# Optimization experiments

Hardware: AMD Instinct MI355X
Metric: run time of the kernel (lower is better)

Reference implementation:

```python
import jax, jax.numpy as jnp
import numpy as np

E, S, G, H, O = 50000, 16, 64, 256, 16


def _mlp(x, W0, b0, W1, b1, W2, b2):
    # x: [..., 2] -> [..., out]
    x = jax.nn.relu(x @ W0 + b0)
    x = jax.nn.relu(x @ W1 + b1)
    return x @ W2 + b2


def setup_inputs() -> dict:
    key = jax.random.key(0)
    ks = jax.random.split(key, 9)
    ob = jax.random.normal(ks[0], (E, S, 3), dtype=jnp.float32)
    action = jax.random.randint(ks[1], (E, S), 0, O).astype(jnp.int64)
    graph_ids = jnp.sort(jax.random.randint(ks[2], (E,), 0, G)).astype(jnp.int32)
    def lin(k, fin, fout):
        return jax.random.normal(k, (fin, fout), dtype=jnp.float32) / jnp.sqrt(jnp.float32(fin))
    return {
        "ob": ob, "action": action, "graph_ids": graph_ids,
        "aW0": lin(ks[3], 2, H), "ab0": jnp.zeros((H,), jnp.float32),
        "aW1": lin(ks[4], H, H), "ab1": jnp.zeros((H,), jnp.float32),
        "aW2": lin(ks[5], H, O), "ab2": jnp.zeros((O,), jnp.float32),
        "cW0": lin(ks[6], 2, H), "cb0": jnp.zeros((H,), jnp.float32),
        "cW1": lin(ks[7], H, H), "cb1": jnp.zeros((H,), jnp.float32),
        "cW2": lin(ks[8], H, 1), "cb2": jnp.zeros((1,), jnp.float32),
    }


def reference(ob, action, graph_ids, aW0, ab0, aW1, ab1, aW2, ab2,
              cW0, cb0, cW1, cb1, cW2, cb2):
    num_edges = ob.shape[0]
    # edge_mask: torch `ob.select(2,0).long() == 0` (truncation toward zero)
    edge_mask = ob[..., 0].astype(jnp.int32) == 0            # [E,S] bool
    mf = edge_mask.astype(ob.dtype)                          # [E,S]
    h = ob[..., 1:3]                                         # [E,S,2]

    # Actor logits over all (edge,sample); mask replaces gather/scatter
    logits = _mlp(h, aW0, ab0, aW1, ab1, aW2, ab2)           # [E,S,O]
    logp = jax.nn.log_softmax(logits, axis=-1)               # [E,S,O]

    # log-prob of given actions, scattered to zeros outside the mask
    alp = jnp.take_along_axis(logp, action[..., None], axis=-1)[..., 0]
    action_log_probs = alp * mf                              # [E,S]

    # critic edge values, scattered to zeros outside the mask
    vals = _mlp(h, cW0, cb0, cW1, cb1, cW2, cb2)[..., 0] * mf  # [E,S]

    # entropy averaged over masked (subgraph) entries only
    ent = -jnp.sum(jnp.exp(logp) * logp, axis=-1)            # [E,S]
    avg_entropy = jnp.sum(ent * mf) / jnp.sum(mf)

    # sum_efeat: per-graph segment sum over edges, divided by num_edges
    value_preds = jax.ops.segment_sum(vals, graph_ids, num_segments=G) / num_edges  # [G,S]

    return action_log_probs, avg_entropy, value_preds, edge_mask
```

## Files before the change

kernel.cpp:

```cpp
#include <hip/hip_runtime.h>
#include <stdint.h>


typedef __attribute__((ext_vector_type(8))) short bf16x8;
typedef __attribute__((ext_vector_type(4))) float f32x4;
typedef __attribute__((ext_vector_type(4))) uint32_t u32x4;

#define NROWS    800000
#define NCHUNK   12500
#define OUT_ENT  800000
#define OUT_VP   800001
#define OUT_MASK 801025

#define SWZ(row) ((((row) & 7) << 4) ^ (((row) & 16) << 1))

__device__ __forceinline__ short f2bf(float x) {
  union { float f; uint32_t u; } v; v.f = x;
  return (short)(uint16_t)((v.u + 0x7FFFu + ((v.u >> 16) & 1u)) >> 16);
}
__device__ __forceinline__ float bf2f(short h) {
  union { uint32_t u; float f; } v; v.u = ((uint32_t)(uint16_t)h) << 16;
  return v.f;
}
template <int C>
__device__ __forceinline__ float dppf(float x) {
  int r = __builtin_amdgcn_update_dpp(0, __builtin_bit_cast(int, x), C, 0xF, 0xF, true);
  return __builtin_bit_cast(float, r);
}
__device__ __forceinline__ float red16_sum(float x) {
  x += dppf<0xB1>(x); x += dppf<0x4E>(x); x += dppf<0x124>(x); x += dppf<0x128>(x); return x;
}
__device__ __forceinline__ float red16_max(float x) {
  x = fmaxf(x, dppf<0xB1>(x)); x = fmaxf(x, dppf<0x4E>(x));
  x = fmaxf(x, dppf<0x124>(x)); x = fmaxf(x, dppf<0x128>(x)); return x;
}
__device__ __forceinline__ uint32_t cvt_pk_bf16(float a, float b) {
  uint32_t r; asm("v_cvt_pk_bf16_f32 %0, %1, %2" : "=v"(r) : "v"(a), "v"(b)); return r;
}

__global__ void zero_kernel(float* out, float* wsf) {
  int t = threadIdx.x + blockIdx.x * blockDim.x;
  for (int i = t; i < 1025; i += 1024) out[OUT_ENT + i] = 0.0f;
  if (t == 0) { wsf[0] = 0.0f; wsf[1] = 0.0f; }
}
__global__ void final_kernel(float* out, const float* wsf) {
  if (threadIdx.x == 0 && blockIdx.x == 0)
    out[OUT_ENT] = (wsf[1] > 0.0f) ? (wsf[0] / wsf[1]) : 0.0f;
}

#define A_ACT1 0
#define A_ACT2 32768
#define A_W2H  65536
#define A_W0   73728
#define A_B0   75776
#define A_OB   76800
#define A_SZ   78848

__global__ void __launch_bounds__(512, 2) ac_actor(
    const float* __restrict__ ob, const int* __restrict__ action,
    const float* __restrict__ aW0, const float* __restrict__ ab0,
    const float* __restrict__ aW1, const float* __restrict__ ab1,
    const float* __restrict__ aW2, const float* __restrict__ ab2,
    float* __restrict__ out, float* __restrict__ wsf)
{
  extern __shared__ char smem[];
  float* w0buf = (float*)(smem + A_W0);
  float* b0buf = (float*)(smem + A_B0);
  float* obufA = (float*)(smem + A_OB);
  const f32x4* w04 = (const f32x4*)(smem + A_W0);
  const f32x4* b04 = (const f32x4*)(smem + A_B0);
  __shared__ float went[8], wmf[8];

  const int tid = threadIdx.x, lane = tid & 63, wave = tid >> 6;
  const int l15 = lane & 15, l4 = lane >> 4;

  w0buf[tid] = aW0[tid];
  if (tid < 256) b0buf[tid] = ab0[tid];
  for (int id = tid; id < 4096; id += 512) {
    int n = id >> 8, k = id & 255;
    *(short*)(smem + A_W2H + n * 512 + ((k * 2) ^ SWZ(n))) = f2bf(aW2[k * 16 + n]);
  }
  const int colbase = wave * 32;
  float b1lane[2] = { ab1[colbase + l15], ab1[colbase + 16 + l15] };
  float b2lane = ab2[l15];
  bf16x8 bh[2][8];
  #pragma unroll
  for (int ct = 0; ct < 2; ++ct) {
    const int n = colbase + ct * 16 + l15;
    #pragma unroll
    for (int ks = 0; ks < 8; ++ks) {
      const int k0 = ks * 32 + 8 * l4;
      bf16x8 h8;
      #pragma unroll
      for (int j = 0; j < 8; ++j) h8[j] = f2bf(aW1[(k0 + j) * 256 + n]);
      bh[ct][ks] = h8;
    }
  }
  const int c0 = blockIdx.x, stride = gridDim.x;
  float sob = 0.0f;
  if (tid < 192) { obufA[tid] = ob[c0 * 192 + tid]; }
  { int cn = c0 + stride; if (cn < NCHUNK && tid < 192) sob = ob[cn * 192 + tid]; }
  __syncthreads();

  float entacc = 0.0f, mfacc = 0.0f;
  int buf = 0;
  for (int c = c0; c < NCHUNK; c += stride, buf ^= 1) {
    const int row0 = c * 64;
    const float* ocur = obufA + buf * 256;
    float* onxt = (float*)(obufA + (buf ^ 1) * 256);

    if (tid < 64) out[OUT_MASK + row0 + tid] = ((int)ocur[tid * 3] == 0) ? 1.0f : 0.0f;
    {
      const int kb = tid & 31;
      f32x4 wa0 = w04[kb * 2], wa1 = w04[kb * 2 + 1];
      f32x4 wb0 = w04[64 + kb * 2], wb1 = w04[64 + kb * 2 + 1];
      f32x4 ba0 = b04[kb * 2], ba1 = b04[kb * 2 + 1];
      #pragma unroll
      for (int i = 0; i < 4; ++i) {
        int row = wave * 2 + 16 * i + (lane >> 5);
        float h0 = ocur[row * 3 + 1], h1 = ocur[row * 3 + 2];
        f32x4 va, vb;
        #pragma unroll
        for (int j = 0; j < 4; ++j) {
          va[j] = fmaxf(fmaf(h0, wa0[j], fmaf(h1, wb0[j], ba0[j])), 0.0f);
          vb[j] = fmaxf(fmaf(h0, wa1[j], fmaf(h1, wb1[j], ba1[j])), 0.0f);
        }
        u32x4 v;
        v[0] = cvt_pk_bf16(va[0], va[1]);
        v[1] = cvt_pk_bf16(va[2], va[3]);
        v[2] = cvt_pk_bf16(vb[0], vb[1]);
        v[3] = cvt_pk_bf16(vb[2], vb[3]);
        *(u32x4*)(smem + A_ACT1 + row * 512 + ((kb * 16) ^ SWZ(row))) = v;
      }
    }
    if (tid < 192) onxt[tid] = sob;
    { int c2 = c + 2 * stride; if (c2 < NCHUNK && tid < 192) sob = ob[c2 * 192 + tid]; }
    __syncthreads();

    const bool evn = (l15 & 1) == 0;
    #pragma unroll 1
    for (int rtp = 0; rtp < 2; ++rtp) {
      f32x4 acc[2][2];
      #pragma unroll
      for (int h = 0; h < 2; ++h)
        #pragma unroll
        for (int ct = 0; ct < 2; ++ct) acc[h][ct] = (f32x4){0.f, 0.f, 0.f, 0.f};
      const int rA0 = rtp * 32 + l15, rA1 = rA0 + 16;
      #pragma unroll
      for (int ks = 0; ks < 8; ++ks) {
        const int cb = ks * 64 + 16 * l4;
        bf16x8 a0 = *(const bf16x8*)(smem + A_ACT1 + rA0 * 512 + (cb ^ SWZ(rA0)));
        bf16x8 a1 = *(const bf16x8*)(smem + A_ACT1 + rA1 * 512 + (cb ^ SWZ(rA1)));
        acc[0][0] = __builtin_amdgcn_mfma_f32_16x16x32_bf16(a0, bh[0][ks], acc[0][0], 0, 0, 0);
        acc[0][1] = __builtin_amdgcn_mfma_f32_16x16x32_bf16(a0, bh[1][ks], acc[0][1], 0, 0, 0);
        acc[1][0] = __builtin_amdgcn_mfma_f32_16x16x32_bf16(a1, bh[0][ks], acc[1][0], 0, 0, 0);
        acc[1][1] = __builtin_amdgcn_mfma_f32_16x16x32_bf16(a1, bh[1][ks], acc[1][1], 0, 0, 0);
      }
      #pragma unroll
      for (int ct = 0; ct < 2; ++ct) {
        const int colb = (colbase + ct * 16 + (l15 & ~1)) * 2;
        #pragma unroll
        for (int r = 0; r < 4; ++r) {
          float v0 = fmaxf(acc[0][ct][r] + b1lane[ct], 0.0f);
          float v1 = fmaxf(acc[1][ct][r] + b1lane[ct], 0.0f);
          float n0 = dppf<0xB1>(v0), n1 = dppf<0xB1>(v1);
          uint32_t w = cvt_pk_bf16(evn ? v0 : n1, evn ? n0 : v1);
          int rr = rtp * 32 + (evn ? 0 : 16) + 4 * l4 + r;
          *(uint32_t*)(smem + A_ACT2 + rr * 512 + (colb ^ SWZ(rr))) = w;
        }
      }
    }
    __syncthreads();

    if (wave < 4) {
      const int rowA = wave * 16 + l15;
      const int swA = SWZ(rowA), swW = SWZ(l15);
      f32x4 ae = {0.f,0.f,0.f,0.f}, ao = {0.f,0.f,0.f,0.f};
      #pragma unroll
      for (int ks = 0; ks < 8; ks += 2) {
        const int cb0 = ks * 64 + 16 * l4, cb1 = cb0 + 64;
        bf16x8 a0 = *(const bf16x8*)(smem + A_ACT2 + rowA * 512 + (cb0 ^ swA));
        bf16x8 a1 = *(const bf16x8*)(smem + A_ACT2 + rowA * 512 + (cb1 ^ swA));
        bf16x8 w0f = *(const bf16x8*)(smem + A_W2H + l15 * 512 + (cb0 ^ swW));
        bf16x8 w1f = *(const bf16x8*)(smem + A_W2H + l15 * 512 + (cb1 ^ swW));
        ae = __builtin_amdgcn_mfma_f32_16x16x32_bf16(a0, w0f, ae, 0, 0, 0);
        ao = __builtin_amdgcn_mfma_f32_16x16x32_bf16(a1, w1f, ao, 0, 0, 0);
      }
      #pragma unroll
      for (int r = 0; r < 4; ++r) {
        const int rl = wave * 16 + 4 * l4 + r;
        float x = ae[r] + ao[r] + b2lane;
        float m = red16_max(x);
        float e = __expf(x - m);
        float s = red16_sum(e);
        float t = red16_sum(e * (x - m));
        float ls = __logf(s);
        float mfr = ((int)ob[(row0 + rl) * 3] == 0) ? 1.0f : 0.0f;
        int av = action[row0 + rl];
        if (l15 == av) out[row0 + rl] = (x - m - ls) * mfr;
        if (l15 == 0) { entacc += (ls - t / s) * mfr; mfacc += mfr; }
      }
    }
  }
  #pragma unroll
  for (int d = 1; d < 64; d <<= 1) { entacc += __shfl_xor(entacc, d); mfacc += __shfl_xor(mfacc, d); }
  if (lane == 0) { went[wave] = entacc; wmf[wave] = mfacc; }
  __syncthreads();
  if (tid == 0) {
    float e = 0.f, m = 0.f;
    #pragma unroll
    for (int i = 0; i < 8; ++i) { e += went[i]; m += wmf[i]; }
    atomicAdd(&wsf[0], e); atomicAdd(&wsf[1], m);
  }
}

#define C_ACT1 0
#define C_W0   32768
#define C_B0   34816
#define C_OB   35840
#define C_VB   37888
#define C_SZ   39936

__global__ void __launch_bounds__(512, 2) ac_critic(
    const float* __restrict__ ob, const int* __restrict__ graph_ids,
    const float* __restrict__ cW0, const float* __restrict__ cb0,
    const float* __restrict__ cW1, const float* __restrict__ cb1,
    const float* __restrict__ cW2, const float* __restrict__ cb2,
    float* __restrict__ out)
{
  extern __shared__ char smem[];
  float* w0buf = (float*)(smem + C_W0);
  float* b0buf = (float*)(smem + C_B0);
  float* obufA = (float*)(smem + C_OB);
  float* vbuf  = (float*)(smem + C_VB);
  const f32x4* w04 = (const f32x4*)(smem + C_W0);
  const f32x4* b04 = (const f32x4*)(smem + C_B0);

  const int tid = threadIdx.x, lane = tid & 63, wave = tid >> 6;
  const int l15 = lane & 15, l4 = lane >> 4;

  w0buf[tid] = cW0[tid];
  if (tid < 256) b0buf[tid] = cb0[tid];
  const float cb2v = cb2[0];
  const int colbase = wave * 32;
  float b1lane[2] = { cb1[colbase + l15], cb1[colbase + 16 + l15] };
  const float w2c0 = cW2[colbase + l15];
  const float w2c1 = cW2[colbase + 16 + l15];

  bf16x8 bh[2][8];
  #pragma unroll
  for (int ct = 0; ct < 2; ++ct) {
    const int n = colbase + ct * 16 + l15;
    #pragma unroll
    for (int ks = 0; ks < 8; ++ks) {
      const int k0 = ks * 32 + 8 * l4;
      bf16x8 h8;
      #pragma unroll
      for (int j = 0; j < 8; ++j) h8[j] = f2bf(cW1[(k0 + j) * 256 + n]);
      bh[ct][ks] = h8;
    }
  }
  const int c0 = blockIdx.x, stride = gridDim.x;
  float sob = 0.0f;
  if (tid < 192) { obufA[tid] = ob[c0 * 192 + tid]; }
  { int cn = c0 + stride; if (cn < NCHUNK && tid < 192) sob = ob[cn * 192 + tid]; }
  __syncthreads();

  int buf = 0;
  for (int c = c0; c < NCHUNK; c += stride, buf ^= 1) {
    const float* ocur = obufA + buf * 256;
    float* onxt = (float*)(obufA + (buf ^ 1) * 256);

    {
      const int kb = tid & 31;
      f32x4 wa0 = w04[kb * 2], wa1 = w04[kb * 2 + 1];
      f32x4 wb0 = w04[64 + kb * 2], wb1 = w04[64 + kb * 2 + 1];
      f32x4 ba0 = b04[kb * 2], ba1 = b04[kb * 2 + 1];
      #pragma unroll
      for (int i = 0; i < 4; ++i) {
        int row = wave * 2 + 16 * i + (lane >> 5);
        float h0 = ocur[row * 3 + 1], h1 = ocur[row * 3 + 2];
        f32x4 va, vb;
        #pragma unroll
        for (int j = 0; j < 4; ++j) {
          va[j] = fmaxf(fmaf(h0, wa0[j], fmaf(h1, wb0[j], ba0[j])), 0.0f);
          vb[j] = fmaxf(fmaf(h0, wa1[j], fmaf(h1, wb1[j], ba1[j])), 0.0f);
        }
        u32x4 v;
        v[0] = cvt_pk_bf16(va[0], va[1]);
        v[1] = cvt_pk_bf16(va[2], va[3]);
        v[2] = cvt_pk_bf16(vb[0], vb[1]);
        v[3] = cvt_pk_bf16(vb[2], vb[3]);
        *(u32x4*)(smem + C_ACT1 + row * 512 + ((kb * 16) ^ SWZ(row))) = v;
      }
    }
    if (tid < 192) onxt[tid] = sob;
    { int c2 = c + 2 * stride; if (c2 < NCHUNK && tid < 192) sob = ob[c2 * 192 + tid]; }
    __syncthreads();

    float o0w0 = 0.0f;
    if (wave == 0) o0w0 = ocur[lane * 3];

    #pragma unroll 1
    for (int rtp = 0; rtp < 2; ++rtp) {
      f32x4 acc[2][2];
      #pragma unroll
      for (int h = 0; h < 2; ++h)
        #pragma unroll
        for (int ct = 0; ct < 2; ++ct) acc[h][ct] = (f32x4){0.f, 0.f, 0.f, 0.f};
      const int rA0 = rtp * 32 + l15, rA1 = rA0 + 16;
      #pragma unroll
      for (int ks = 0; ks < 8; ++ks) {
        const int cb = ks * 64 + 16 * l4;
        bf16x8 a0 = *(const bf16x8*)(smem + C_ACT1 + rA0 * 512 + (cb ^ SWZ(rA0)));
        bf16x8 a1 = *(const bf16x8*)(smem + C_ACT1 + rA1 * 512 + (cb ^ SWZ(rA1)));
        acc[0][0] = __builtin_amdgcn_mfma_f32_16x16x32_bf16(a0, bh[0][ks], acc[0][0], 0, 0, 0);
        acc[0][1] = __builtin_amdgcn_mfma_f32_16x16x32_bf16(a0, bh[1][ks], acc[0][1], 0, 0, 0);
        acc[1][0] = __builtin_amdgcn_mfma_f32_16x16x32_bf16(a1, bh[0][ks], acc[1][0], 0, 0, 0);
        acc[1][1] = __builtin_amdgcn_mfma_f32_16x16x32_bf16(a1, bh[1][ks], acc[1][1], 0, 0, 0);
      }
      #pragma unroll
      for (int h = 0; h < 2; ++h) {
        #pragma unroll
        for (int r = 0; r < 4; ++r) {
          float p = fmaxf(acc[h][0][r] + b1lane[0], 0.0f) * w2c0
                  + fmaxf(acc[h][1][r] + b1lane[1], 0.0f) * w2c1;
          p = red16_sum(p);
          if (l15 == 0) vbuf[wave * 64 + rtp * 32 + h * 16 + 4 * l4 + r] = p;
        }
      }
    }
    __syncthreads();

    if (wave == 0) {
      float v = 0.0f;
      #pragma unroll
      for (int w = 0; w < 8; ++w) v += vbuf[w * 64 + lane];
      if ((int)o0w0 == 0) {
        int g = graph_ids[c * 4 + (lane >> 4)];
        atomicAdd(&out[OUT_VP + g * 16 + (lane & 15)], (v + cb2v) * (1.0f / 50000.0f));
      }
    }
  }
}

extern "C" void kernel_launch(void* const* d_in, const int* in_sizes, int n_in,
                              void* d_out, int out_size, void* d_ws, size_t ws_size,
                              hipStream_t stream) {
  const float* ob     = (const float*)d_in[0];
  const int*   action = (const int*)d_in[1];
  const int*   gids   = (const int*)d_in[2];
  const float* aW0 = (const float*)d_in[3],  *ab0 = (const float*)d_in[4];
  const float* aW1 = (const float*)d_in[5],  *ab1 = (const float*)d_in[6];
  const float* aW2 = (const float*)d_in[7],  *ab2 = (const float*)d_in[8];
  const float* cW0 = (const float*)d_in[9],  *cb0 = (const float*)d_in[10];
  const float* cW1 = (const float*)d_in[11], *cb1 = (const float*)d_in[12];
  const float* cW2 = (const float*)d_in[13], *cb2 = (const float*)d_in[14];
  float* out = (float*)d_out;
  float* wsf = (float*)d_ws;

  zero_kernel<<<2, 512, 0, stream>>>(out, wsf);
  ac_actor<<<512, 512, A_SZ, stream>>>(ob, action, aW0, ab0, aW1, ab1, aW2, ab2, out, wsf);
  ac_critic<<<512, 512, C_SZ, stream>>>(ob, gids, cW0, cb0, cW1, cb1, cW2, cb2, out);
  final_kernel<<<1, 64, 0, stream>>>(out, wsf);
}
```

Before: 502.6 us.

## Merge actor and critic kernels into one launch with role-split blocks

```diff
diff --git a/kernel.cpp b/kernel.cpp
--- a/kernel.cpp
+++ b/kernel.cpp
@@ -48,41 +48,61 @@
     out[OUT_ENT] = (wsf[1] > 0.0f) ? (wsf[0] / wsf[1]) : 0.0f;
 }
 
-#define A_ACT1 0
-#define A_ACT2 32768
-#define A_W2H  65536
-#define A_W0   73728
-#define A_B0   75776
-#define A_OB   76800
-#define A_SZ   78848
-
-__global__ void __launch_bounds__(512, 2) ac_actor(
+#define L_ACT1 0
+#define L_ACT2 32768
+#define L_W2H  65536
+#define L_W0   73728
+#define L_B0   75776
+#define L_OB   76800
+#define L_SZ   78848
+
+__global__ void __launch_bounds__(512, 2) ac_main(
     const float* __restrict__ ob, const int* __restrict__ action,
+    const int* __restrict__ graph_ids,
     const float* __restrict__ aW0, const float* __restrict__ ab0,
     const float* __restrict__ aW1, const float* __restrict__ ab1,
     const float* __restrict__ aW2, const float* __restrict__ ab2,
+    const float* __restrict__ cW0, const float* __restrict__ cb0,
+    const float* __restrict__ cW1, const float* __restrict__ cb1,
+    const float* __restrict__ cW2, const float* __restrict__ cb2,
     float* __restrict__ out, float* __restrict__ wsf)
 {
   extern __shared__ char smem[];
-  float* w0buf = (float*)(smem + A_W0);
-  float* b0buf = (float*)(smem + A_B0);
-  float* obufA = (float*)(smem + A_OB);
-  const f32x4* w04 = (const f32x4*)(smem + A_W0);
-  const f32x4* b04 = (const f32x4*)(smem + A_B0);
+  float* w0buf = (float*)(smem + L_W0);
+  float* b0buf = (float*)(smem + L_B0);
+  float* obufA = (float*)(smem + L_OB);
+  float* vbuf  = (float*)(smem + L_ACT2);
+  const f32x4* w04 = (const f32x4*)(smem + L_W0);
+  const f32x4* b04 = (const f32x4*)(smem + L_B0);
   __shared__ float went[8], wmf[8];
+
+  const int b = blockIdx.x;
+  const int role = (b >> 8) & 1;
+  const int pid  = (b & 255) | ((b >> 9) << 8);
+  const int stride = 512;
 
   const int tid = threadIdx.x, lane = tid & 63, wave = tid >> 6;
   const int l15 = lane & 15, l4 = lane >> 4;
 
-  w0buf[tid] = aW0[tid];
-  if (tid < 256) b0buf[tid] = ab0[tid];
-  for (int id = tid; id < 4096; id += 512) {
-    int n = id >> 8, k = id & 255;
-    *(short*)(smem + A_W2H + n * 512 + ((k * 2) ^ SWZ(n))) = f2bf(aW2[k * 16 + n]);
+  const float* W0s = role ? cW0 : aW0;
+  const float* B0s = role ? cb0 : ab0;
+  const float* W1s = role ? cW1 : aW1;
+  const float* B1s = role ? cb1 : ab1;
+
+  w0buf[tid] = W0s[tid];
+  if (tid < 256) b0buf[tid] = B0s[tid];
+  if (!role) {
+    for (int id = tid; id < 4096; id += 512) {
+      int n = id >> 8, k = id & 255;
+      *(short*)(smem + L_W2H + n * 512 + ((k * 2) ^ SWZ(n))) = f2bf(aW2[k * 16 + n]);
+    }
   }
   const int colbase = wave * 32;
-  float b1lane[2] = { ab1[colbase + l15], ab1[colbase + 16 + l15] };
-  float b2lane = ab2[l15];
+  float b1lane[2] = { B1s[colbase + l15], B1s[colbase + 16 + l15] };
+  float b2lane = 0.0f, w2c0 = 0.0f, w2c1 = 0.0f, cb2v = 0.0f;
+  if (!role) b2lane = ab2[l15];
+  else { w2c0 = cW2[colbase + l15]; w2c1 = cW2[colbase + 16 + l15]; cb2v = cb2[0]; }
+
   bf16x8 bh[2][8];
   #pragma unroll
   for (int ct = 0; ct < 2; ++ct) {
@@ -92,24 +112,24 @@
       const int k0 = ks * 32 + 8 * l4;
       bf16x8 h8;
       #pragma unroll
-      for (int j = 0; j < 8; ++j) h8[j] = f2bf(aW1[(k0 + j) * 256 + n]);
+      for (int j = 0; j < 8; ++j) h8[j] = f2bf(W1s[(k0 + j) * 256 + n]);
       bh[ct][ks] = h8;
     }
   }
-  const int c0 = blockIdx.x, stride = gridDim.x;
   float sob = 0.0f;
-  if (tid < 192) { obufA[tid] = ob[c0 * 192 + tid]; }
-  { int cn = c0 + stride; if (cn < NCHUNK && tid < 192) sob = ob[cn * 192 + tid]; }
+  if (tid < 192) { obufA[tid] = ob[pid * 192 + tid]; }
+  { int cn = pid + stride; if (cn < NCHUNK && tid < 192) sob = ob[cn * 192 + tid]; }
   __syncthreads();
 
   float entacc = 0.0f, mfacc = 0.0f;
   int buf = 0;
-  for (int c = c0; c < NCHUNK; c += stride, buf ^= 1) {
+  for (int c = pid; c < NCHUNK; c += stride, buf ^= 1) {
     const int row0 = c * 64;
     const float* ocur = obufA + buf * 256;
     float* onxt = (float*)(obufA + (buf ^ 1) * 256);
 
-    if (tid < 64) out[OUT_MASK + row0 + tid] = ((int)ocur[tid * 3] == 0) ? 1.0f : 0.0f;
+    if (!role && tid < 64)
+      out[OUT_MASK + row0 + tid] = ((int)ocur[tid * 3] == 0) ? 1.0f : 0.0f;
     {
       const int kb = tid & 31;
       f32x4 wa0 = w04[kb * 2], wa1 = w04[kb * 2 + 1];
@@ -130,12 +150,15 @@
         v[1] = cvt_pk_bf16(va[2], va[3]);
         v[2] = cvt_pk_bf16(vb[0], vb[1]);
         v[3] = cvt_pk_bf16(vb[2], vb[3]);
-        *(u32x4*)(smem + A_ACT1 + row * 512 + ((kb * 16) ^ SWZ(row))) = v;
+        *(u32x4*)(smem + L_ACT1 + row * 512 + ((kb * 16) ^ SWZ(row))) = v;
       }
     }
     if (tid < 192) onxt[tid] = sob;
     { int c2 = c + 2 * stride; if (c2 < NCHUNK && tid < 192) sob = ob[c2 * 192 + tid]; }
     __syncthreads();
+
+    float o0w0 = 0.0f;
+    if (role && wave == 0) o0w0 = ocur[lane * 3];
 
     const bool evn = (l15 & 1) == 0;
     #pragma unroll 1
@@ -144,52 +167,68 @@
       #pragma unroll
       for (int h = 0; h < 2; ++h)
         #pragma unroll
-        for (int ct = 0; ct < 2; ++ct) acc[h][ct] = (f32x4){0.f, 0.f, 0.f, 0.f};
+        for (int ct = 0; ct < 2; ++ct)
+          acc[h][ct] = (f32x4){b1lane[ct], b1lane[ct], b1lane[ct], b1lane[ct]};
       const int rA0 = rtp * 32 + l15, rA1 = rA0 + 16;
       #pragma unroll
       for (int ks = 0; ks < 8; ++ks) {
         const int cb = ks * 64 + 16 * l4;
-        bf16x8 a0 = *(const bf16x8*)(smem + A_ACT1 + rA0 * 512 + (cb ^ SWZ(rA0)));
-        bf16x8 a1 = *(const bf16x8*)(smem + A_ACT1 + rA1 * 512 + (cb ^ SWZ(rA1)));
+        bf16x8 a0 = *(const bf16x8*)(smem + L_ACT1 + rA0 * 512 + (cb ^ SWZ(rA0)));
+        bf16x8 a1 = *(const bf16x8*)(smem + L_ACT1 + rA1 * 512 + (cb ^ SWZ(rA1)));
         acc[0][0] = __builtin_amdgcn_mfma_f32_16x16x32_bf16(a0, bh[0][ks], acc[0][0], 0, 0, 0);
         acc[0][1] = __builtin_amdgcn_mfma_f32_16x16x32_bf16(a0, bh[1][ks], acc[0][1], 0, 0, 0);
         acc[1][0] = __builtin_amdgcn_mfma_f32_16x16x32_bf16(a1, bh[0][ks], acc[1][0], 0, 0, 0);
         acc[1][1] = __builtin_amdgcn_mfma_f32_16x16x32_bf16(a1, bh[1][ks], acc[1][1], 0, 0, 0);
       }
-      #pragma unroll
-      for (int ct = 0; ct < 2; ++ct) {
-        const int colb = (colbase + ct * 16 + (l15 & ~1)) * 2;
-        #pragma unroll
-        for (int r = 0; r < 4; ++r) {
-          float v0 = fmaxf(acc[0][ct][r] + b1lane[ct], 0.0f);
-          float v1 = fmaxf(acc[1][ct][r] + b1lane[ct], 0.0f);
-          float n0 = dppf<0xB1>(v0), n1 = dppf<0xB1>(v1);
-          uint32_t w = cvt_pk_bf16(evn ? v0 : n1, evn ? n0 : v1);
-          int rr = rtp * 32 + (evn ? 0 : 16) + 4 * l4 + r;
-          *(uint32_t*)(smem + A_ACT2 + rr * 512 + (colb ^ SWZ(rr))) = w;
+      if (!role) {
+        #pragma unroll
+        for (int ct = 0; ct < 2; ++ct) {
+          const int colb = (colbase + ct * 16 + (l15 & ~1)) * 2;
+          #pragma unroll
+          for (int r = 0; r < 4; ++r) {
+            float v0 = fmaxf(acc[0][ct][r], 0.0f);
+            float v1 = fmaxf(acc[1][ct][r], 0.0f);
+            float n0 = dppf<0xB1>(v0), n1 = dppf<0xB1>(v1);
+            uint32_t w = cvt_pk_bf16(evn ? v0 : n1, evn ? n0 : v1);
+            int rr = rtp * 32 + (evn ? 0 : 16) + 4 * l4 + r;
+            *(uint32_t*)(smem + L_ACT2 + rr * 512 + (colb ^ SWZ(rr))) = w;
+          }
+        }
+      } else {
+        #pragma unroll
+        for (int h = 0; h < 2; ++h) {
+          #pragma unroll
+          for (int r = 0; r < 4; ++r) {
+            float p = fmaxf(acc[h][0][r], 0.0f) * w2c0
+                    + fmaxf(acc[h][1][r], 0.0f) * w2c1;
+            p = red16_sum(p);
+            if (l15 == 0) vbuf[wave * 64 + rtp * 32 + h * 16 + 4 * l4 + r] = p;
+          }
         }
       }
     }
     __syncthreads();
 
-    if (wave < 4) {
-      const int rowA = wave * 16 + l15;
+    if (!role) {
+      const int rt = wave & 3, half = wave >> 2;
+      const int rowA = rt * 16 + l15;
       const int swA = SWZ(rowA), swW = SWZ(l15);
-      f32x4 ae = {0.f,0.f,0.f,0.f}, ao = {0.f,0.f,0.f,0.f};
+      f32x4 ae = {b2lane, b2lane, b2lane, b2lane}, ao = {0.f,0.f,0.f,0.f};
       #pragma unroll
       for (int ks = 0; ks < 8; ks += 2) {
         const int cb0 = ks * 64 + 16 * l4, cb1 = cb0 + 64;
-        bf16x8 a0 = *(const bf16x8*)(smem + A_ACT2 + rowA * 512 + (cb0 ^ swA));
-        bf16x8 a1 = *(const bf16x8*)(smem + A_ACT2 + rowA * 512 + (cb1 ^ swA));
-        bf16x8 w0f = *(const bf16x8*)(smem + A_W2H + l15 * 512 + (cb0 ^ swW));
-        bf16x8 w1f = *(const bf16x8*)(smem + A_W2H + l15 * 512 + (cb1 ^ swW));
+        bf16x8 a0 = *(const bf16x8*)(smem + L_ACT2 + rowA * 512 + (cb0 ^ swA));
+        bf16x8 a1 = *(const bf16x8*)(smem + L_ACT2 + rowA * 512 + (cb1 ^ swA));
+        bf16x8 w0f = *(const bf16x8*)(smem + L_W2H + l15 * 512 + (cb0 ^ swW));
+        bf16x8 w1f = *(const bf16x8*)(smem + L_W2H + l15 * 512 + (cb1 ^ swW));
         ae = __builtin_amdgcn_mfma_f32_16x16x32_bf16(a0, w0f, ae, 0, 0, 0);
         ao = __builtin_amdgcn_mfma_f32_16x16x32_bf16(a1, w1f, ao, 0, 0, 0);
       }
       #pragma unroll
-      for (int r = 0; r < 4; ++r) {
-        const int rl = wave * 16 + 4 * l4 + r;
-        float x = ae[r] + ao[r] + b2lane;
+      for (int r2 = 0; r2 < 2; ++r2) {
+        const int r = half * 2 + r2;
+        const int rl = rt * 16 + 4 * l4 + r;
+        float x = ae[r] + ao[r];
         float m = red16_max(x);
         float e = __expf(x - m);
         float s = red16_sum(e);
@@ -200,146 +239,28 @@
         if (l15 == av) out[row0 + rl] = (x - m - ls) * mfr;
         if (l15 == 0) { entacc += (ls - t / s) * mfr; mfacc += mfr; }
       }
-    }
-  }
-  #pragma unroll
-  for (int d = 1; d < 64; d <<= 1) { entacc += __shfl_xor(entacc, d); mfacc += __shfl_xor(mfacc, d); }
-  if (lane == 0) { went[wave] = entacc; wmf[wave] = mfacc; }
-  __syncthreads();
-  if (tid == 0) {
-    float e = 0.f, m = 0.f;
+    } else {
+      if (wave == 0) {
+        float v = 0.0f;
+        #pragma unroll
+        for (int w = 0; w < 8; ++w) v += vbuf[w * 64 + lane];
+        if ((int)o0w0 == 0) {
+          int g = graph_ids[c * 4 + (lane >> 4)];
+          atomicAdd(&out[OUT_VP + g * 16 + (lane & 15)], (v + cb2v) * (1.0f / 50000.0f));
+        }
+      }
+    }
+  }
+  if (!role) {
     #pragma unroll
-    for (int i = 0; i < 8; ++i) { e += went[i]; m += wmf[i]; }
-    atomicAdd(&wsf[0], e); atomicAdd(&wsf[1], m);
-  }
-}
-
-#define C_ACT1 0
-#define C_W0   32768
-#define C_B0   34816
-#define C_OB   35840
-#define C_VB   37888
-#define C_SZ   39936
-
-__global__ void __launch_bounds__(512, 2) ac_critic(
-    const float* __restrict__ ob, const int* __restrict__ graph_ids,
-    const float* __restrict__ cW0, const float* __restrict__ cb0,
-    const float* __restrict__ cW1, const float* __restrict__ cb1,
-    const float* __restrict__ cW2, const float* __restrict__ cb2,
-    float* __restrict__ out)
-{
-  extern __shared__ char smem[];
-  float* w0buf = (float*)(smem + C_W0);
-  float* b0buf = (float*)(smem + C_B0);
-  float* obufA = (float*)(smem + C_OB);
-  float* vbuf  = (float*)(smem + C_VB);
-  const f32x4* w04 = (const f32x4*)(smem + C_W0);
-  const f32x4* b04 = (const f32x4*)(smem + C_B0);
-
-  const int tid = threadIdx.x, lane = tid & 63, wave = tid >> 6;
-  const int l15 = lane & 15, l4 = lane >> 4;
-
-  w0buf[tid] = cW0[tid];
-  if (tid < 256) b0buf[tid] = cb0[tid];
-  const float cb2v = cb2[0];
-  const int colbase = wave * 32;
-  float b1lane[2] = { cb1[colbase + l15], cb1[colbase + 16 + l15] };
-  const float w2c0 = cW2[colbase + l15];
-  const float w2c1 = cW2[colbase + 16 + l15];
-
-  bf16x8 bh[2][8];
-  #pragma unroll
-  for (int ct = 0; ct < 2; ++ct) {
-    const int n = colbase + ct * 16 + l15;
-    #pragma unroll
-    for (int ks = 0; ks < 8; ++ks) {
-      const int k0 = ks * 32 + 8 * l4;
-      bf16x8 h8;
-      #pragma unroll
-      for (int j = 0; j < 8; ++j) h8[j] = f2bf(cW1[(k0 + j) * 256 + n]);
-      bh[ct][ks] = h8;
-    }
-  }
-  const int c0 = blockIdx.x, stride = gridDim.x;
-  float sob = 0.0f;
-  if (tid < 192) { obufA[tid] = ob[c0 * 192 + tid]; }
-  { int cn = c0 + stride; if (cn < NCHUNK && tid < 192) sob = ob[cn * 192 + tid]; }
-  __syncthreads();
-
-  int buf = 0;
-  for (int c = c0; c < NCHUNK; c += stride, buf ^= 1) {
-    const float* ocur = obufA + buf * 256;
-    float* onxt = (float*)(obufA + (buf ^ 1) * 256);
-
-    {
-      const int kb = tid & 31;
-      f32x4 wa0 = w04[kb * 2], wa1 = w04[kb * 2 + 1];
-      f32x4 wb0 = w04[64 + kb * 2], wb1 = w04[64 + kb * 2 + 1];
-      f32x4 ba0 = b04[kb * 2], ba1 = b04[kb * 2 + 1];
-      #pragma unroll
-      for (int i = 0; i < 4; ++i) {
-        int row = wave * 2 + 16 * i + (lane >> 5);
-        float h0 = ocur[row * 3 + 1], h1 = ocur[row * 3 + 2];
-        f32x4 va, vb;
-        #pragma unroll
-        for (int j = 0; j < 4; ++j) {
-          va[j] = fmaxf(fmaf(h0, wa0[j], fmaf(h1, wb0[j], ba0[j])), 0.0f);
-          vb[j] = fmaxf(fmaf(h0, wa1[j], fmaf(h1, wb1[j], ba1[j])), 0.0f);
-        }
-        u32x4 v;
-        v[0] = cvt_pk_bf16(va[0], va[1]);
-        v[1] = cvt_pk_bf16(va[2], va[3]);
-        v[2] = cvt_pk_bf16(vb[0], vb[1]);
-        v[3] = cvt_pk_bf16(vb[2], vb[3]);
-        *(u32x4*)(smem + C_ACT1 + row * 512 + ((kb * 16) ^ SWZ(row))) = v;
-      }
-    }
-    if (tid < 192) onxt[tid] = sob;
-    { int c2 = c + 2 * stride; if (c2 < NCHUNK && tid < 192) sob = ob[c2 * 192 + tid]; }
+    for (int d = 1; d < 64; d <<= 1) { entacc += __shfl_xor(entacc, d); mfacc += __shfl_xor(mfacc, d); }
+    if (lane == 0) { went[wave] = entacc; wmf[wave] = mfacc; }
     __syncthreads();
-
-    float o0w0 = 0.0f;
-    if (wave == 0) o0w0 = ocur[lane * 3];
-
-    #pragma unroll 1
-    for (int rtp = 0; rtp < 2; ++rtp) {
-      f32x4 acc[2][2];
-      #pragma unroll
-      for (int h = 0; h < 2; ++h)
-        #pragma unroll
-        for (int ct = 0; ct < 2; ++ct) acc[h][ct] = (f32x4){0.f, 0.f, 0.f, 0.f};
-      const int rA0 = rtp * 32 + l15, rA1 = rA0 + 16;
-      #pragma unroll
-      for (int ks = 0; ks < 8; ++ks) {
-        const int cb = ks * 64 + 16 * l4;
-        bf16x8 a0 = *(const bf16x8*)(smem + C_ACT1 + rA0 * 512 + (cb ^ SWZ(rA0)));
-        bf16x8 a1 = *(const bf16x8*)(smem + C_ACT1 + rA1 * 512 + (cb ^ SWZ(rA1)));
-        acc[0][0] = __builtin_amdgcn_mfma_f32_16x16x32_bf16(a0, bh[0][ks], acc[0][0], 0, 0, 0);
-        acc[0][1] = __builtin_amdgcn_mfma_f32_16x16x32_bf16(a0, bh[1][ks], acc[0][1], 0, 0, 0);
-        acc[1][0] = __builtin_amdgcn_mfma_f32_16x16x32_bf16(a1, bh[0][ks], acc[1][0], 0, 0, 0);
-        acc[1][1] = __builtin_amdgcn_mfma_f32_16x16x32_bf16(a1, bh[1][ks], acc[1][1], 0, 0, 0);
-      }
-      #pragma unroll
-      for (int h = 0; h < 2; ++h) {
-        #pragma unroll
-        for (int r = 0; r < 4; ++r) {
-          float p = fmaxf(acc[h][0][r] + b1lane[0], 0.0f) * w2c0
-                  + fmaxf(acc[h][1][r] + b1lane[1], 0.0f) * w2c1;
-          p = red16_sum(p);
-          if (l15 == 0) vbuf[wave * 64 + rtp * 32 + h * 16 + 4 * l4 + r] = p;
-        }
-      }
-    }
-    __syncthreads();
-
-    if (wave == 0) {
-      float v = 0.0f;
-      #pragma unroll
-      for (int w = 0; w < 8; ++w) v += vbuf[w * 64 + lane];
-      if ((int)o0w0 == 0) {
-        int g = graph_ids[c * 4 + (lane >> 4)];
-        atomicAdd(&out[OUT_VP + g * 16 + (lane & 15)], (v + cb2v) * (1.0f / 50000.0f));
-      }
+    if (tid == 0) {
+      float e = 0.f, m = 0.f;
+      #pragma unroll
+      for (int i = 0; i < 8; ++i) { e += went[i]; m += wmf[i]; }
+      atomicAdd(&wsf[0], e); atomicAdd(&wsf[1], m);
     }
   }
 }
@@ -360,7 +281,7 @@
   float* wsf = (float*)d_ws;
 
   zero_kernel<<<2, 512, 0, stream>>>(out, wsf);
-  ac_actor<<<512, 512, A_SZ, stream>>>(ob, action, aW0, ab0, aW1, ab1, aW2, ab2, out, wsf);
-  ac_critic<<<512, 512, C_SZ, stream>>>(ob, gids, cW0, cb0, cW1, cb1, cW2, cb2, out);
+  ac_main<<<1024, 512, L_SZ, stream>>>(ob, action, gids, aW0, ab0, aW1, ab1, aW2, ab2,
+                                       cW0, cb0, cW1, cb1, cW2, cb2, out, wsf);
   final_kernel<<<1, 64, 0, stream>>>(out, wsf);
 }
```

Measured after the change: 479.5 us. 1.05x faster.
